# Optimization experiments

Hardware: AMD Instinct MI355X
Metric: run time of the kernel (lower is better)

The kernel has to match this reference:

```python
import jax, jax.numpy as jnp
import numpy as np

B, C, H, W = 32, 256, 56, 56
KS, NK = 7, 16
EPS = 1e-5

def setup_inputs() -> dict:
    key = jax.random.key(0)
    ks = jax.random.split(key, 9)
    return {
        "x": jax.random.normal(ks[0], (B, C, H, W), jnp.float32),
        "bn_gamma": jax.random.normal(ks[1], (C,), jnp.float32) * 0.1 + 1.0,
        "bn_beta": jax.random.normal(ks[2], (C,), jnp.float32) * 0.1,
        "bn_mean": jax.random.normal(ks[3], (C,), jnp.float32) * 0.1,
        "bn_var": jax.random.uniform(ks[4], (C,), jnp.float32) + 0.5,
        "q_w": jax.random.normal(ks[5], (C, C), jnp.float32) / np.sqrt(C),
        "k_w": jax.random.normal(ks[6], (NK, C), jnp.float32) / np.sqrt(C),
        "kernel_bank": jax.random.normal(ks[7], (NK, KS * KS), jnp.float32),
        "bias": jnp.zeros((C,), jnp.float32),
    }

def reference(x, bn_gamma, bn_beta, bn_mean, bn_var, q_w, k_w, kernel_bank, bias):
    b, c, h, w = x.shape
    temp = 2.0 * c  # self.temp = channels * 2
    # BatchNorm2d (eval mode: affine with running stats)
    scale = bn_gamma / jnp.sqrt(bn_var + EPS)
    xn = (x - bn_mean[:, None, None]) * scale[:, None, None] + bn_beta[:, None, None]
    xf = xn.reshape(b, c, h * w)                       # [B, C, HW]
    Q = jnp.einsum('oc,bcn->bon', q_w, xf)             # 1x1 conv -> [B, C, HW]
    K = jnp.einsum('kc,bcn->bnk', k_w, xf)             # 1x1 conv -> [B, HW, NK]
    attn = jax.nn.softmax(jnp.einsum('bcn,bnk->bck', Q, K) / temp, axis=2)  # [B, C, NK]
    wgt = jnp.einsum('bck,ke->bce', attn, kernel_bank)  # [B, C, KS*KS]
    wgt = wgt.reshape(b * c, 1, KS, KS)                # per-sample per-channel kernels
    pad = KS // 2
    # dynamic depthwise conv: groups = B*C  (torch padding='same')
    out = jax.lax.conv_general_dilated(
        x.reshape(1, b * c, h, w), wgt,
        window_strides=(1, 1), padding=[(pad, pad), (pad, pad)],
        feature_group_count=b * c,
        dimension_numbers=('NCHW', 'OIHW', 'NCHW'))
    return out.reshape(b, c, h, w) + bias[None, :, None, None]
```

## Files before the change

### kernel.cpp

```cpp
#include <hip/hip_runtime.h>
#include <hip/hip_bf16.h>

#define BATCH 32
#define CH    256
#define HWPX  3136
#define WIDTH 56
#define NK    16
#define NSLAB 28
#define NSUB  4
#define WGTS  52
#define EPSV  1e-5f

__device__ __forceinline__ unsigned pk_bf2(float a, float b) {
    __hip_bfloat16 ha = __float2bfloat16(a), hb = __float2bfloat16(b);
    unsigned short ua = *reinterpret_cast<unsigned short*>(&ha);
    unsigned short ub = *reinterpret_cast<unsigned short*>(&hb);
    return ((unsigned)ub << 16) | ua;
}
__device__ __forceinline__ float up_lo(unsigned v) { return __uint_as_float(v << 16); }
__device__ __forceinline__ float up_hi(unsigned v) { return __uint_as_float(v & 0xffff0000u); }

__global__ __launch_bounds__(64) void kkvec(
    const float* __restrict__ x,
    const float* __restrict__ gamma, const float* __restrict__ beta,
    const float* __restrict__ mean,  const float* __restrict__ var,
    const float* __restrict__ kw,    unsigned short* __restrict__ Kpart)
{
    const int sub = blockIdx.x / 784;
    const int pb  = blockIdx.x % 784;
    const int job = pb * 64 + threadIdx.x;
    const int b   = job / 1568;
    const int px2 = job % 1568;
    const int cbase = sub * 64;
    const float* xp = x + ((size_t)b * CH + cbase) * HWPX + px2 * 2;

    float acc0[NK], acc1[NK];
#pragma unroll
    for (int k = 0; k < NK; ++k) { acc0[k] = 0.f; acc1[k] = 0.f; }

    for (int c0 = 0; c0 < 64; c0 += 8) {
        float2 v[8];
#pragma unroll
        for (int i = 0; i < 8; ++i)
            v[i] = *(const float2*)(xp + (size_t)(c0 + i) * HWPX);
#pragma unroll
        for (int i = 0; i < 8; ++i) {
            const int c = cbase + c0 + i;
            const float sc = gamma[c] * rsqrtf(var[c] + EPSV);
            const float sh = fmaf(-mean[c], sc, beta[c]);
            v[i].x = fmaf(v[i].x, sc, sh);
            v[i].y = fmaf(v[i].y, sc, sh);
        }
#pragma unroll
        for (int k = 0; k < NK; ++k) {
            const float4 w0 = *(const float4*)(kw + k * CH + cbase + c0);
            const float4 w1 = *(const float4*)(kw + k * CH + cbase + c0 + 4);
            acc0[k] = fmaf(v[0].x, w0.x, acc0[k]); acc1[k] = fmaf(v[0].y, w0.x, acc1[k]);
            acc0[k] = fmaf(v[1].x, w0.y, acc0[k]); acc1[k] = fmaf(v[1].y, w0.y, acc1[k]);
            acc0[k] = fmaf(v[2].x, w0.z, acc0[k]); acc1[k] = fmaf(v[2].y, w0.z, acc1[k]);
            acc0[k] = fmaf(v[3].x, w0.w, acc0[k]); acc1[k] = fmaf(v[3].y, w0.w, acc1[k]);
            acc0[k] = fmaf(v[4].x, w1.x, acc0[k]); acc1[k] = fmaf(v[4].y, w1.x, acc1[k]);
            acc0[k] = fmaf(v[5].x, w1.y, acc0[k]); acc1[k] = fmaf(v[5].y, w1.y, acc1[k]);
            acc0[k] = fmaf(v[6].x, w1.z, acc0[k]); acc1[k] = fmaf(v[6].y, w1.z, acc1[k]);
            acc0[k] = fmaf(v[7].x, w1.w, acc0[k]); acc1[k] = fmaf(v[7].y, w1.w, acc1[k]);
        }
    }

    unsigned short* op = Kpart + ((size_t)sub * BATCH * HWPX + (size_t)b * HWPX + px2 * 2) * NK;
    uint4* op4 = (uint4*)op;
    op4[0] = make_uint4(pk_bf2(acc0[0],  acc0[1]),  pk_bf2(acc0[2],  acc0[3]),
                        pk_bf2(acc0[4],  acc0[5]),  pk_bf2(acc0[6],  acc0[7]));
    op4[1] = make_uint4(pk_bf2(acc0[8],  acc0[9]),  pk_bf2(acc0[10], acc0[11]),
                        pk_bf2(acc0[12], acc0[13]), pk_bf2(acc0[14], acc0[15]));
    op4[2] = make_uint4(pk_bf2(acc1[0],  acc1[1]),  pk_bf2(acc1[2],  acc1[3]),
                        pk_bf2(acc1[4],  acc1[5]),  pk_bf2(acc1[6],  acc1[7]));
    op4[3] = make_uint4(pk_bf2(acc1[8],  acc1[9]),  pk_bf2(acc1[10], acc1[11]),
                        pk_bf2(acc1[12], acc1[13]), pk_bf2(acc1[14], acc1[15]));
}

__global__ __launch_bounds__(256) void ksum(
    const unsigned short* __restrict__ Kpart, float* __restrict__ Kbuf)
{
    const int i = blockIdx.x * 256 + threadIdx.x;
    const uint2* p = (const uint2*)Kpart;
    float4 s = make_float4(0.f, 0.f, 0.f, 0.f);
#pragma unroll
    for (int s2 = 0; s2 < NSUB; ++s2) {
        const uint2 v = p[(size_t)s2 * 401408 + i];
        s.x += up_lo(v.x); s.y += up_hi(v.x);
        s.z += up_lo(v.y); s.w += up_hi(v.y);
    }
    ((float4*)Kbuf)[i] = s;
}

__global__ __launch_bounds__(256) void kpmat(
    const float* __restrict__ x,
    const float* __restrict__ gamma, const float* __restrict__ beta,
    const float* __restrict__ mean,  const float* __restrict__ var,
    const float* __restrict__ Kbuf,  float* __restrict__ Pp)
{
    const int b  = blockIdx.x / NSLAB;
    const int nb = blockIdx.x % NSLAB;
    const int n0 = nb * 112;
    const int c  = threadIdx.x;

    const float sc = gamma[c] * rsqrtf(var[c] + EPSV);
    const float sh = fmaf(-mean[c], sc, beta[c]);

    const float4* xr = (const float4*)(x + ((size_t)b * CH + c) * HWPX + n0);
    const float*  Kp = Kbuf + ((size_t)b * HWPX + n0) * NK;

    float acc[NK];
#pragma unroll
    for (int k = 0; k < NK; ++k) acc[k] = 0.f;

#pragma unroll 4
    for (int j = 0; j < 28; ++j) {
        const float4 xv = xr[j];
        float v[4];
        v[0] = fmaf(xv.x, sc, sh); v[1] = fmaf(xv.y, sc, sh);
        v[2] = fmaf(xv.z, sc, sh); v[3] = fmaf(xv.w, sc, sh);
#pragma unroll
        for (int d = 0; d < 4; ++d) {
            const float vd = v[d];
#pragma unroll
            for (int kq = 0; kq < 4; ++kq) {
                const float4 kv = *(const float4*)(Kp + ((j*4 + d) * NK) + kq*4);
                acc[kq*4+0] = fmaf(vd, kv.x, acc[kq*4+0]);
                acc[kq*4+1] = fmaf(vd, kv.y, acc[kq*4+1]);
                acc[kq*4+2] = fmaf(vd, kv.z, acc[kq*4+2]);
                acc[kq*4+3] = fmaf(vd, kv.w, acc[kq*4+3]);
            }
        }
    }
    float4* op = (float4*)(Pp + (((size_t)b * NSLAB + nb) * CH + c) * NK);
#pragma unroll
    for (int kq = 0; kq < 4; ++kq)
        op[kq] = make_float4(acc[kq*4+0], acc[kq*4+1], acc[kq*4+2], acc[kq*4+3]);
}

__global__ __launch_bounds__(256) void kpred(
    const float* __restrict__ Pp, float* __restrict__ P)
{
    const int idx = blockIdx.x * 256 + threadIdx.x;
    const int b = idx >> 12;
    const int e = idx & 4095;
    const float* p = Pp + (size_t)b * NSLAB * 4096 + e;
    float s = 0.f;
#pragma unroll
    for (int nb = 0; nb < NSLAB; ++nb) s += p[(size_t)nb * 4096];
    P[idx] = s;
}

__global__ __launch_bounds__(256) void ksoft(
    const float* __restrict__ P, const float* __restrict__ qw,
    const float* __restrict__ bank, float* __restrict__ wgt)
{
    const int b  = blockIdx.x >> 3;
    const int cb = blockIdx.x & 7;
    const int tid = threadIdx.x;

    __shared__ float s_P[CH * NK];
    __shared__ float s_red[32 * 8 * NK];
    __shared__ float s_S[32 * NK];
    __shared__ float s_attn[32 * NK];

    for (int idx = tid; idx < CH * NK; idx += 256)
        s_P[idx] = P[(size_t)b * CH * NK + idx];
    __syncthreads();

    const int c_l = tid & 31, sub = tid >> 5;
    const int c = cb * 32 + c_l;
    float a[NK];
#pragma unroll
    for (int k = 0; k < NK; ++k) a[k] = 0.f;
    const float* qrow = qw + (size_t)c * CH + sub * 32;
    for (int j = 0; j < 32; ++j) {
        const float qv = qrow[j];
        const float4* p4 = (const float4*)&s_P[(sub * 32 + j) * NK];
#pragma unroll
        for (int kq = 0; kq < 4; ++kq) {
            const float4 pv = p4[kq];
            a[kq*4+0] = fmaf(qv, pv.x, a[kq*4+0]);
            a[kq*4+1] = fmaf(qv, pv.y, a[kq*4+1]);
            a[kq*4+2] = fmaf(qv, pv.z, a[kq*4+2]);
            a[kq*4+3] = fmaf(qv, pv.w, a[kq*4+3]);
        }
    }
#pragma unroll
    for (int kq = 0; kq < 4; ++kq)
        *(float4*)&s_red[(c_l * 8 + sub) * NK + kq*4] =
            make_float4(a[kq*4+0], a[kq*4+1], a[kq*4+2], a[kq*4+3]);
    __syncthreads();

    for (int idx = tid; idx < 32 * NK; idx += 256) {
        const int cl = idx >> 4, k = idx & 15;
        float s = 0.f;
#pragma unroll
        for (int s2 = 0; s2 < 8; ++s2) s += s_red[(cl * 8 + s2) * NK + k];
        s_S[idx] = s * (1.f / 512.f);
    }
    __syncthreads();

    if (tid < 32) {
        float l[NK];
#pragma unroll
        for (int k = 0; k < NK; ++k) l[k] = s_S[tid * NK + k];
        float m = l[0];
#pragma unroll
        for (int k = 1; k < NK; ++k) m = fmaxf(m, l[k]);
        float sum = 0.f;
#pragma unroll
        for (int k = 0; k < NK; ++k) { l[k] = __expf(l[k] - m); sum += l[k]; }
        const float inv = 1.f / sum;
#pragma unroll
        for (int k = 0; k < NK; ++k) s_attn[tid * NK + k] = l[k] * inv;
    }
    __syncthreads();

    for (int idx = tid; idx < 32 * 49; idx += 256) {
        const int cl = idx / 49, e = idx - cl * 49;
        float wv = 0.f;
#pragma unroll
        for (int k = 0; k < NK; ++k)
            wv = fmaf(s_attn[cl * NK + k], bank[k * 49 + e], wv);
        wgt[((size_t)b * CH + cb * 32 + cl) * WGTS + e] = wv;
    }
}

__global__ __launch_bounds__(256) void kconv(
    const float* __restrict__ x, const float* __restrict__ wgt,
    const float* __restrict__ bias, float* __restrict__ out)
{
    const int t  = threadIdx.x;
    const int pl = t >> 4;
    const int q  = t & 15;
    const int qc = q < 14 ? q : 13;
    const int h  = blockIdx.x & 1;
    const int plane = (blockIdx.x >> 1) * 16 + pl;
    const int ho = h * 28;
    const bool qlo = (q == 0), qhi = (q >= 13);
    const float bv = bias[plane & 255];

    float4 wv[13];
    const float4* wp4 = (const float4*)(wgt + (size_t)plane * WGTS);
#pragma unroll
    for (int i = 0; i < 13; ++i) wv[i] = wp4[i];
#define WTAP(idx) ((idx)%4==0 ? wv[(idx)/4].x : (idx)%4==1 ? wv[(idx)/4].y : \
                   (idx)%4==2 ? wv[(idx)/4].z : wv[(idx)/4].w)

    const float* xrow = x   + (size_t)plane * HWPX + 4 * qc;
    float*       orow = out + (size_t)plane * HWPX + 4 * qc;

    float a[7][4];
#pragma unroll
    for (int i = 0; i < 7; ++i)
#pragma unroll
        for (int ix = 0; ix < 4; ++ix) a[i][ix] = bv;

    const float4 z4 = make_float4(0.f, 0.f, 0.f, 0.f);
    int ir0 = ho - 3;
    float4 vc = (0 <= ir0 && ir0 < 56) ? *(const float4*)(xrow + ir0 * WIDTH) : z4;

#pragma unroll 7
    for (int j = 0; j < 35; ++j) {
        const int snew = j % 7;
#pragma unroll
        for (int ix = 0; ix < 4; ++ix) a[snew][ix] = bv;

        const int irn = ho - 3 + j + 1;
        float4 vn = (0 <= irn && irn < 56 && j + 1 < 35)
                        ? *(const float4*)(xrow + irn * WIDTH) : z4;

        float rr1 = __shfl_up(vc.y, 1), rr2 = __shfl_up(vc.z, 1), rr3 = __shfl_up(vc.w, 1);
        float rr8 = __shfl_down(vc.x, 1), rr9 = __shfl_down(vc.y, 1), rr10 = __shfl_down(vc.z, 1);
        float rr[11];
        rr[1] = qlo ? 0.f : rr1;  rr[2] = qlo ? 0.f : rr2;  rr[3] = qlo ? 0.f : rr3;
        rr[4] = vc.x; rr[5] = vc.y; rr[6] = vc.z; rr[7] = vc.w;
        rr[8] = qhi ? 0.f : rr8;  rr[9] = qhi ? 0.f : rr9;  rr[10] = qhi ? 0.f : rr10;

#pragma unroll
        for (int i = 0; i < 7; ++i) {
            const int ky = 6 - i;
            const int s  = (j + i + 1) % 7;
#pragma unroll
            for (int kx = 0; kx < 7; ++kx) {
                const float wk = WTAP(ky * 7 + kx);
#pragma unroll
                for (int ix = 0; ix < 4; ++ix)
                    a[s][ix] = fmaf(wk, rr[ix + kx + 1], a[s][ix]);
            }
        }

        if (j >= 6 && j < 34) {
            const int o  = ho + j - 6;
            const int sd = (j + 1) % 7;
            if (q < 14)
                *(float4*)(orow + o * WIDTH) =
                    make_float4(a[sd][0], a[sd][1], a[sd][2], a[sd][3]);
        }
        vc = vn;
    }
#undef WTAP
}

extern "C" void kernel_launch(void* const* d_in, const int* in_sizes, int n_in,
                              void* d_out, int out_size, void* d_ws, size_t ws_size,
                              hipStream_t stream)
{
    const float* x     = (const float*)d_in[0];
    const float* gamma = (const float*)d_in[1];
    const float* beta  = (const float*)d_in[2];
    const float* mean  = (const float*)d_in[3];
    const float* var   = (const float*)d_in[4];
    const float* qw    = (const float*)d_in[5];
    const float* kw    = (const float*)d_in[6];
    const float* bank  = (const float*)d_in[7];
    const float* bias  = (const float*)d_in[8];
    float* out = (float*)d_out;

    const size_t KBUF_F = (size_t)BATCH * HWPX * NK;
    const size_t PP_F   = (size_t)BATCH * NSLAB * CH * NK;

    float* ws    = (float*)d_ws;
    float* Kbuf  = ws;
    unsigned short* Kpart = (unsigned short*)(ws + KBUF_F);
    float* Pp    = ws + KBUF_F;
    float* P     = ws + KBUF_F + PP_F;
    float* wgt   = P + (size_t)BATCH * CH * NK;

    kkvec<<<dim3(NSUB * 784),   dim3(64),  0, stream>>>(x, gamma, beta, mean, var, kw, Kpart);
    ksum <<<dim3(1568),         dim3(256), 0, stream>>>(Kpart, Kbuf);
    kpmat<<<dim3(BATCH * NSLAB),dim3(256), 0, stream>>>(x, gamma, beta, mean, var, Kbuf, Pp);
    kpred<<<dim3(512),          dim3(256), 0, stream>>>(Pp, P);
    ksoft<<<dim3(BATCH * 8),    dim3(256), 0, stream>>>(P, qw, bank, wgt);
    kconv<<<dim3(BATCH * CH / 8), dim3(256), 0, stream>>>(x, wgt, bias, out);
}
```

Measured before the change: 131.3 us.

## Restage K-projection through LDS, store conv weights as bf16, split conv rows further

The K-projection kernel now loads 64 channels x 64 pixels per block into shared memory (with BN applied) and has each thread compute one pixel, rather than each thread streaming two pixels straight from global memory. The per-plane dynamic conv weights are stored as bf16 with a padded stride, so each conv thread loads 28 registers instead of 52 floats. The depthwise conv now splits each plane into four 14-row chunks instead of two 28-row chunks, giving more blocks at the cost of more halo-row reloads. The bf16 weights add rounding error to the output.

```diff
diff --git a/kernel.cpp b/kernel.cpp
--- a/kernel.cpp
+++ b/kernel.cpp
@@ -8,7 +8,7 @@
 #define NK    16
 #define NSLAB 28
 #define NSUB  4
-#define WGTS  52
+#define WGTS  56
 #define EPSV  1e-5f
 
 __device__ __forceinline__ unsigned pk_bf2(float a, float b) {
@@ -17,6 +17,10 @@
     unsigned short ub = *reinterpret_cast<unsigned short*>(&hb);
     return ((unsigned)ub << 16) | ua;
 }
+__device__ __forceinline__ unsigned short bf16u(float f) {
+    __hip_bfloat16 h = __float2bfloat16(f);
+    return *reinterpret_cast<unsigned short*>(&h);
+}
 __device__ __forceinline__ float up_lo(unsigned v) { return __uint_as_float(v << 16); }
 __device__ __forceinline__ float up_hi(unsigned v) { return __uint_as_float(v & 0xffff0000u); }
 
@@ -26,56 +30,61 @@
     const float* __restrict__ mean,  const float* __restrict__ var,
     const float* __restrict__ kw,    unsigned short* __restrict__ Kpart)
 {
-    const int sub = blockIdx.x / 784;
-    const int pb  = blockIdx.x % 784;
-    const int job = pb * 64 + threadIdx.x;
-    const int b   = job / 1568;
-    const int px2 = job % 1568;
-    const int cbase = sub * 64;
-    const float* xp = x + ((size_t)b * CH + cbase) * HWPX + px2 * 2;
-
-    float acc0[NK], acc1[NK];
-#pragma unroll
-    for (int k = 0; k < NK; ++k) { acc0[k] = 0.f; acc1[k] = 0.f; }
-
-    for (int c0 = 0; c0 < 64; c0 += 8) {
-        float2 v[8];
-#pragma unroll
-        for (int i = 0; i < 8; ++i)
-            v[i] = *(const float2*)(xp + (size_t)(c0 + i) * HWPX);
-#pragma unroll
-        for (int i = 0; i < 8; ++i) {
-            const int c = cbase + c0 + i;
-            const float sc = gamma[c] * rsqrtf(var[c] + EPSV);
-            const float sh = fmaf(-mean[c], sc, beta[c]);
-            v[i].x = fmaf(v[i].x, sc, sh);
-            v[i].y = fmaf(v[i].y, sc, sh);
-        }
-#pragma unroll
-        for (int k = 0; k < NK; ++k) {
-            const float4 w0 = *(const float4*)(kw + k * CH + cbase + c0);
-            const float4 w1 = *(const float4*)(kw + k * CH + cbase + c0 + 4);
-            acc0[k] = fmaf(v[0].x, w0.x, acc0[k]); acc1[k] = fmaf(v[0].y, w0.x, acc1[k]);
-            acc0[k] = fmaf(v[1].x, w0.y, acc0[k]); acc1[k] = fmaf(v[1].y, w0.y, acc1[k]);
-            acc0[k] = fmaf(v[2].x, w0.z, acc0[k]); acc1[k] = fmaf(v[2].y, w0.z, acc1[k]);
-            acc0[k] = fmaf(v[3].x, w0.w, acc0[k]); acc1[k] = fmaf(v[3].y, w0.w, acc1[k]);
-            acc0[k] = fmaf(v[4].x, w1.x, acc0[k]); acc1[k] = fmaf(v[4].y, w1.x, acc1[k]);
-            acc0[k] = fmaf(v[5].x, w1.y, acc0[k]); acc1[k] = fmaf(v[5].y, w1.y, acc1[k]);
-            acc0[k] = fmaf(v[6].x, w1.z, acc0[k]); acc1[k] = fmaf(v[6].y, w1.z, acc1[k]);
-            acc0[k] = fmaf(v[7].x, w1.w, acc0[k]); acc1[k] = fmaf(v[7].y, w1.w, acc1[k]);
-        }
-    }
-
-    unsigned short* op = Kpart + ((size_t)sub * BATCH * HWPX + (size_t)b * HWPX + px2 * 2) * NK;
-    uint4* op4 = (uint4*)op;
-    op4[0] = make_uint4(pk_bf2(acc0[0],  acc0[1]),  pk_bf2(acc0[2],  acc0[3]),
-                        pk_bf2(acc0[4],  acc0[5]),  pk_bf2(acc0[6],  acc0[7]));
-    op4[1] = make_uint4(pk_bf2(acc0[8],  acc0[9]),  pk_bf2(acc0[10], acc0[11]),
-                        pk_bf2(acc0[12], acc0[13]), pk_bf2(acc0[14], acc0[15]));
-    op4[2] = make_uint4(pk_bf2(acc1[0],  acc1[1]),  pk_bf2(acc1[2],  acc1[3]),
-                        pk_bf2(acc1[4],  acc1[5]),  pk_bf2(acc1[6],  acc1[7]));
-    op4[3] = make_uint4(pk_bf2(acc1[8],  acc1[9]),  pk_bf2(acc1[10], acc1[11]),
-                        pk_bf2(acc1[12], acc1[13]), pk_bf2(acc1[14], acc1[15]));
+    const int blk = blockIdx.x;
+    const int sub = blk / 1568;
+    const int rem = blk - sub * 1568;
+    const int b   = rem / 49;
+    const int t   = rem - b * 49;
+    const int n0  = t * 64;
+    const int lane = threadIdx.x;
+
+    __shared__ float s_x[64 * 65];
+
+    {
+        const int ch = sub * 64 + lane;
+        const float sc = gamma[ch] * rsqrtf(var[ch] + EPSV);
+        const float sh = fmaf(-mean[ch], sc, beta[ch]);
+        const float4* xr = (const float4*)(x + ((size_t)b * CH + ch) * HWPX + n0);
+        float* dst = s_x + lane * 65;
+#pragma unroll
+        for (int j = 0; j < 16; ++j) {
+            const float4 v = xr[j];
+            dst[4*j+0] = fmaf(v.x, sc, sh);
+            dst[4*j+1] = fmaf(v.y, sc, sh);
+            dst[4*j+2] = fmaf(v.z, sc, sh);
+            dst[4*j+3] = fmaf(v.w, sc, sh);
+        }
+    }
+    __syncthreads();
+
+    {
+        const int p = lane;
+        float acc[NK];
+#pragma unroll
+        for (int k = 0; k < NK; ++k) acc[k] = 0.f;
+#pragma unroll 4
+        for (int c0 = 0; c0 < 64; c0 += 4) {
+            const float xv0 = s_x[(c0+0)*65 + p];
+            const float xv1 = s_x[(c0+1)*65 + p];
+            const float xv2 = s_x[(c0+2)*65 + p];
+            const float xv3 = s_x[(c0+3)*65 + p];
+#pragma unroll
+            for (int k = 0; k < NK; ++k) {
+                const float4 k4 = *(const float4*)(kw + k * CH + sub * 64 + c0);
+                acc[k] = fmaf(xv0, k4.x, acc[k]);
+                acc[k] = fmaf(xv1, k4.y, acc[k]);
+                acc[k] = fmaf(xv2, k4.z, acc[k]);
+                acc[k] = fmaf(xv3, k4.w, acc[k]);
+            }
+        }
+        unsigned short* op = Kpart +
+            ((size_t)sub * BATCH * HWPX + (size_t)b * HWPX + n0 + p) * NK;
+        uint4* op4 = (uint4*)op;
+        op4[0] = make_uint4(pk_bf2(acc[0],  acc[1]),  pk_bf2(acc[2],  acc[3]),
+                            pk_bf2(acc[4],  acc[5]),  pk_bf2(acc[6],  acc[7]));
+        op4[1] = make_uint4(pk_bf2(acc[8],  acc[9]),  pk_bf2(acc[10], acc[11]),
+                            pk_bf2(acc[12], acc[13]), pk_bf2(acc[14], acc[15]));
+    }
 }
 
 __global__ __launch_bounds__(256) void ksum(
@@ -154,7 +163,7 @@
 
 __global__ __launch_bounds__(256) void ksoft(
     const float* __restrict__ P, const float* __restrict__ qw,
-    const float* __restrict__ bank, float* __restrict__ wgt)
+    const float* __restrict__ bank, unsigned short* __restrict__ wgt)
 {
     const int b  = blockIdx.x >> 3;
     const int cb = blockIdx.x & 7;
@@ -224,30 +233,33 @@
 #pragma unroll
         for (int k = 0; k < NK; ++k)
             wv = fmaf(s_attn[cl * NK + k], bank[k * 49 + e], wv);
-        wgt[((size_t)b * CH + cb * 32 + cl) * WGTS + e] = wv;
+        wgt[((size_t)b * CH + cb * 32 + cl) * WGTS + e] = bf16u(wv);
     }
 }
 
 __global__ __launch_bounds__(256) void kconv(
-    const float* __restrict__ x, const float* __restrict__ wgt,
+    const float* __restrict__ x, const unsigned short* __restrict__ wgt,
     const float* __restrict__ bias, float* __restrict__ out)
 {
     const int t  = threadIdx.x;
     const int pl = t >> 4;
     const int q  = t & 15;
     const int qc = q < 14 ? q : 13;
-    const int h  = blockIdx.x & 1;
-    const int plane = (blockIdx.x >> 1) * 16 + pl;
-    const int ho = h * 28;
+    const int h  = blockIdx.x & 3;
+    const int plane = (blockIdx.x >> 2) * 16 + pl;
+    const int ho = h * 14;
     const bool qlo = (q == 0), qhi = (q >= 13);
     const float bv = bias[plane & 255];
 
-    float4 wv[13];
-    const float4* wp4 = (const float4*)(wgt + (size_t)plane * WGTS);
-#pragma unroll
-    for (int i = 0; i < 13; ++i) wv[i] = wp4[i];
-#define WTAP(idx) ((idx)%4==0 ? wv[(idx)/4].x : (idx)%4==1 ? wv[(idx)/4].y : \
-                   (idx)%4==2 ? wv[(idx)/4].z : wv[(idx)/4].w)
+    unsigned wu[28];
+    const uint4* wp4 = (const uint4*)(wgt + (size_t)plane * WGTS);
+#pragma unroll
+    for (int i = 0; i < 7; ++i) {
+        const uint4 v = wp4[i];
+        wu[4*i+0] = v.x; wu[4*i+1] = v.y; wu[4*i+2] = v.z; wu[4*i+3] = v.w;
+    }
+#define WTAP(idx) __uint_as_float(((idx) & 1) ? (wu[(idx)>>1] & 0xffff0000u) \
+                                              : (wu[(idx)>>1] << 16))
 
     const float* xrow = x   + (size_t)plane * HWPX + 4 * qc;
     float*       orow = out + (size_t)plane * HWPX + 4 * qc;
@@ -263,13 +275,13 @@
     float4 vc = (0 <= ir0 && ir0 < 56) ? *(const float4*)(xrow + ir0 * WIDTH) : z4;
 
 #pragma unroll 7
-    for (int j = 0; j < 35; ++j) {
+    for (int j = 0; j < 21; ++j) {
         const int snew = j % 7;
 #pragma unroll
         for (int ix = 0; ix < 4; ++ix) a[snew][ix] = bv;
 
         const int irn = ho - 3 + j + 1;
-        float4 vn = (0 <= irn && irn < 56 && j + 1 < 35)
+        float4 vn = (0 <= irn && irn < 56 && j + 1 < 21)
                         ? *(const float4*)(xrow + irn * WIDTH) : z4;
 
         float rr1 = __shfl_up(vc.y, 1), rr2 = __shfl_up(vc.z, 1), rr3 = __shfl_up(vc.w, 1);
@@ -292,7 +304,7 @@
             }
         }
 
-        if (j >= 6 && j < 34) {
+        if (j >= 6 && j < 20) {
             const int o  = ho + j - 6;
             const int sd = (j + 1) % 7;
             if (q < 14)
@@ -327,12 +339,12 @@
     unsigned short* Kpart = (unsigned short*)(ws + KBUF_F);
     float* Pp    = ws + KBUF_F;
     float* P     = ws + KBUF_F + PP_F;
-    float* wgt   = P + (size_t)BATCH * CH * NK;
-
-    kkvec<<<dim3(NSUB * 784),   dim3(64),  0, stream>>>(x, gamma, beta, mean, var, kw, Kpart);
-    ksum <<<dim3(1568),         dim3(256), 0, stream>>>(Kpart, Kbuf);
-    kpmat<<<dim3(BATCH * NSLAB),dim3(256), 0, stream>>>(x, gamma, beta, mean, var, Kbuf, Pp);
-    kpred<<<dim3(512),          dim3(256), 0, stream>>>(Pp, P);
-    ksoft<<<dim3(BATCH * 8),    dim3(256), 0, stream>>>(P, qw, bank, wgt);
-    kconv<<<dim3(BATCH * CH / 8), dim3(256), 0, stream>>>(x, wgt, bias, out);
-}
+    unsigned short* wgt = (unsigned short*)(P + (size_t)BATCH * CH * NK);
+
+    kkvec<<<dim3(NSUB * BATCH * 49), dim3(64),  0, stream>>>(x, gamma, beta, mean, var, kw, Kpart);
+    ksum <<<dim3(1568),              dim3(256), 0, stream>>>(Kpart, Kbuf);
+    kpmat<<<dim3(BATCH * NSLAB),     dim3(256), 0, stream>>>(x, gamma, beta, mean, var, Kbuf, Pp);
+    kpred<<<dim3(512),               dim3(256), 0, stream>>>(Pp, P);
+    ksoft<<<dim3(BATCH * 8),         dim3(256), 0, stream>>>(P, qw, bank, wgt);
+    kconv<<<dim3(BATCH * CH / 4),    dim3(256), 0, stream>>>(x, wgt, bias, out);
+}
```

Result: slower. 155.9 us (+18.7%).
